# Performance work log

Hardware: AMD Instinct MI355X
Metric: run time of the kernel (lower is better)

The kernel has to match this reference:

```python
import jax, jax.numpy as jnp
import numpy as np

D_MODEL = 1024
H = 16
D_K = D_MODEL // H  # 64
B, S = 2, 2048


def setup_inputs() -> dict:
    key = jax.random.key(0)
    ks = jax.random.split(key, 8)
    scale = 1.0 / np.sqrt(D_MODEL)
    return {
        "q": jax.random.normal(ks[0], (B, S, D_MODEL), dtype=jnp.float32),
        "k": jax.random.normal(ks[1], (B, S, D_MODEL), dtype=jnp.float32),
        "v": jax.random.normal(ks[2], (B, S, D_MODEL), dtype=jnp.float32),
        "W_q": jax.random.normal(ks[3], (H, D_MODEL, D_K), dtype=jnp.float32) * scale,
        "W_k": jax.random.normal(ks[4], (H, D_MODEL, D_K), dtype=jnp.float32) * scale,
        "W_v": jax.random.normal(ks[5], (H, D_MODEL, D_K), dtype=jnp.float32) * scale,
        "W_o": jax.random.normal(ks[6], (D_MODEL, H * D_K), dtype=jnp.float32) * scale,
        "b_o": jnp.zeros((D_MODEL,), dtype=jnp.float32),
    }


def reference(q, k, v, W_q, W_k, W_v, W_o, b_o):
    b, s, _ = q.shape
    h, _, d_k = W_q.shape
    inv_sqrt_dk = jnp.asarray(1.0 / np.sqrt(d_k), q.dtype)
    # per-head projections: [b, h, s, d_k]
    qh = jnp.einsum("bsd,hdk->bhsk", q, W_q)
    kh = jnp.einsum("bsd,hdk->bhsk", k, W_k)
    vh = jnp.einsum("bsd,hdk->bhsk", v, W_v)
    # scaled dot product attention
    scores = jnp.einsum("bhqk,bhsk->bhqs", qh, kh) * inv_sqrt_dk  # [b,h,S,S]
    attn = jax.nn.softmax(scores, axis=-1)
    ctx = jnp.einsum("bhqs,bhsk->bhqk", attn, vh)  # [b,h,S,d_k]
    # chunk over heads + concat along feature dim -> [b, S, h*d_k], head-major
    ctx = ctx.transpose(0, 2, 1, 3).reshape(b, s, h * d_k)
    # final linear
    return ctx @ W_o.T + b_o
```

## Files before the change

### kernel.cpp

```cpp
#include <hip/hip_runtime.h>
#include <cstdint>
#include <cstddef>


typedef unsigned short bf16_t;
typedef __attribute__((ext_vector_type(8))) short short8;
typedef __attribute__((ext_vector_type(4))) float f32x4;

__device__ __forceinline__ uint32_t fbits(float f) {
  union { float f; uint32_t u; } v; v.f = f; return v.u;
}
__device__ __forceinline__ bf16_t f2bf(float f) {
  uint32_t u = fbits(f);
  return (bf16_t)((u + 0x7FFFu + ((u >> 16) & 1u)) >> 16);
}
__device__ __forceinline__ uint32_t packbf2(float lo, float hi) {
  uint32_t a = fbits(hi) + 0x8000u;
  uint32_t b = fbits(lo) + 0x8000u;
  return __builtin_amdgcn_perm(a, b, 0x07060302u);
}
__device__ __forceinline__ int4 cvt8(f32x4 lo, f32x4 hi) {
  return make_int4((int)packbf2(lo.x, lo.y), (int)packbf2(lo.z, lo.w),
                   (int)packbf2(hi.x, hi.y), (int)packbf2(hi.z, hi.w));
}

__global__ void prep_kernel(const float* __restrict__ Wo,
                            const float* __restrict__ Wq, const float* __restrict__ Wk,
                            const float* __restrict__ Wv,
                            bf16_t* __restrict__ Woo,
                            bf16_t* __restrict__ Wtq, bf16_t* __restrict__ Wtk,
                            bf16_t* __restrict__ Wtv) {
  int blk = blockIdx.x;
  int tid = threadIdx.x;
  if (blk < 1024) {
    int i = blk * 256 + tid;
    f32x4 val = ((const f32x4*)Wo)[i];
    ushort4 o;
    o.x = f2bf(val.x); o.y = f2bf(val.y); o.z = f2bf(val.z); o.w = f2bf(val.w);
    ((ushort4*)Woo)[i] = o;
  } else {
    int blk2 = blk - 1024;
    int z = blk2 >> 9, t = blk2 & 511;
    const float* W = z == 0 ? Wq : z == 1 ? Wk : Wv;
    bf16_t* Wt = z == 0 ? Wtq : z == 1 ? Wtk : Wtv;
    int h = t >> 5, d0 = (t & 31) * 32;
    __shared__ float tile[32][65];
    const float* src = W + ((size_t)h << 16) + (size_t)d0 * 64;
    int d = tid >> 3;
#pragma unroll
    for (int j = 0; j < 2; j++) {
      int dk = (tid & 7) * 8 + j * 4;
      *(f32x4*)&tile[d][dk] = *(const f32x4*)(src + d * 64 + dk);
    }
    __syncthreads();
    int dk2 = tid >> 2, c = tid & 3;
    union { ushort s[8]; int4 v; } o;
#pragma unroll
    for (int j = 0; j < 8; j++) o.s[j] = f2bf(tile[c * 8 + j][dk2]);
    *(int4*)(Wt + (size_t)(h * 64 + dk2) * 1024 + d0 + c * 8) = o.v;
  }
}

__global__ __launch_bounds__(256) void gemm_proj_kernel(
    const float* __restrict__ A0, const float* __restrict__ A1, const float* __restrict__ A2,
    const bf16_t* __restrict__ B0, const bf16_t* __restrict__ B1, const bf16_t* __restrict__ B2,
    bf16_t* __restrict__ O0, bf16_t* __restrict__ O1, bf16_t* __restrict__ O2,
    float s0)
{
  const int bid = blockIdx.x;
  const int nIdx = bid / 96;
  const int g = bid - nIdx * 96;
  const int z = g % 3;
  const int m0 = (g / 3) * 128, n0 = nIdx * 128;

  const float* A   = z == 0 ? A0 : z == 1 ? A1 : A2;
  const bf16_t* Bt = z == 0 ? B0 : z == 1 ? B1 : B2;
  bf16_t* Cout     = z == 0 ? O0 : z == 1 ? O1 : O2;
  const float scale = z == 0 ? s0 : 1.0f;
  const int K = 1024;

  __shared__ alignas(16) bf16_t smem[18432];

  const int tid = threadIdx.x;
  const int lane = tid & 63, wave = tid >> 6;
  const int wm = wave >> 1, wn = wave & 1;
  const int quad = lane >> 4, l15 = lane & 15;

  f32x4 acc[4][4];
#pragma unroll
  for (int i = 0; i < 4; i++)
#pragma unroll
    for (int j = 0; j < 4; j++) acc[i][j] = (f32x4)0.0f;

  const int c0 = wave * 128 + lane;
  const int c1 = c0 + 64;
  const float*  pa0 = A  + (size_t)(m0 + (c0 >> 2)) * K + (c0 & 3) * 8;
  const float*  pa1 = A  + (size_t)(m0 + (c1 >> 2)) * K + (c1 & 3) * 8;
  const bf16_t* pb0 = Bt + (size_t)(n0 + (c0 >> 2)) * K + (c0 & 3) * 8;
  const bf16_t* pb1 = Bt + (size_t)(n0 + (c1 >> 2)) * K + (c1 & 3) * 8;
  const int s0a = c0 * 8, s1a = c1 * 8;

  f32x4 ra0l = *(const f32x4*)pa0, ra0h = *(const f32x4*)(pa0 + 4);
  f32x4 ra1l = *(const f32x4*)pa1, ra1h = *(const f32x4*)(pa1 + 4);
  int4 rb0 = *(const int4*)pb0;
  int4 rb1 = *(const int4*)pb1;
  *(int4*)(smem + s0a) = cvt8(ra0l, ra0h);
  *(int4*)(smem + s1a) = cvt8(ra1l, ra1h);
  *(int4*)(smem + 4096 + s0a) = rb0;
  *(int4*)(smem + 4096 + s1a) = rb1;
  __syncthreads();

  for (int it = 0; it < 32; ++it) {
    const int co = (it & 1) * 8192;
    if (it < 31) {
      const int ko = (it + 1) * 32;
      ra0l = *(const f32x4*)(pa0 + ko); ra0h = *(const f32x4*)(pa0 + ko + 4);
      ra1l = *(const f32x4*)(pa1 + ko); ra1h = *(const f32x4*)(pa1 + ko + 4);
      rb0 = *(const int4*)(pb0 + ko);
      rb1 = *(const int4*)(pb1 + ko);
    }

    short8 af[4], bfr[4];
#pragma unroll
    for (int mi = 0; mi < 4; mi++)
      af[mi] = *(const short8*)(smem + co + (wm * 64 + mi * 16 + l15) * 32 + quad * 8);
#pragma unroll
    for (int ni = 0; ni < 4; ni++)
      bfr[ni] = *(const short8*)(smem + co + 4096 + (wn * 64 + ni * 16 + l15) * 32 + quad * 8);
#pragma unroll
    for (int mi = 0; mi < 4; mi++)
#pragma unroll
      for (int ni = 0; ni < 4; ni++)
        acc[mi][ni] = __builtin_amdgcn_mfma_f32_16x16x32_bf16(af[mi], bfr[ni], acc[mi][ni], 0, 0, 0);

    if (it < 31) {
      const int no = ((it + 1) & 1) * 8192;
      *(int4*)(smem + no + s0a) = cvt8(ra0l, ra0h);
      *(int4*)(smem + no + s1a) = cvt8(ra1l, ra1h);
      *(int4*)(smem + no + 4096 + s0a) = rb0;
      *(int4*)(smem + no + 4096 + s1a) = rb1;
    }
    __syncthreads();
  }

  const int s0r = m0 & 2047, bb = m0 >> 11, hp = n0 >> 6;
  if (z < 2) {
    bf16_t* slot = smem + wn * 9216;
#pragma unroll
    for (int ni = 0; ni < 4; ni++)
#pragma unroll
      for (int mi = 0; mi < 4; mi++)
#pragma unroll
        for (int r = 0; r < 4; r++)
          slot[(wm * 64 + mi * 16 + quad * 4 + r) * 72 + ni * 16 + l15] =
              f2bf(acc[mi][ni][r] * scale);
    __syncthreads();
#pragma unroll
    for (int rd = 0; rd < 8; ++rd) {
      int idx = rd * 256 + tid;
      int si = idx >> 10, mm = (idx >> 3) & 127, c8 = idx & 7;
      int4 val = *(const int4*)(smem + si * 9216 + mm * 72 + c8 * 8);
      *(int4*)(Cout + ((size_t)((bb * 16 + hp + si) * 2048 + s0r + mm)) * 64 + c8 * 8) = val;
    }
  } else {
    bf16_t* slot = smem + wn * 8704;
#pragma unroll
    for (int ni = 0; ni < 4; ni++)
#pragma unroll
      for (int mi = 0; mi < 4; mi++) {
        uint2 pk = make_uint2(packbf2(acc[mi][ni][0], acc[mi][ni][1]),
                              packbf2(acc[mi][ni][2], acc[mi][ni][3]));
        *(uint2*)(slot + (ni * 16 + l15) * 136 + wm * 64 + mi * 16 + quad * 4) = pk;
      }
    __syncthreads();
#pragma unroll
    for (int rd = 0; rd < 8; ++rd) {
      int idx = rd * 256 + tid;
      int si = idx >> 10, c = (idx >> 4) & 63, ck = idx & 15;
      int4 val = *(const int4*)(smem + si * 8704 + c * 136 + ck * 8);
      *(int4*)(Cout + (size_t)(bb * 16 + hp + si) * 131072 + (size_t)c * 2048 + s0r + ck * 8) = val;
    }
  }
}

__global__ __launch_bounds__(256) void gemm_out_kernel(
    const bf16_t* __restrict__ A, const bf16_t* __restrict__ Bt,
    float* __restrict__ C, const float* __restrict__ bias)
{
  const int K = 1024, N = 1024;
  __shared__ alignas(16) bf16_t smem[12288];
  const int tid = threadIdx.x;
  const int lane = tid & 63, wave = tid >> 6;
  const int quad = lane >> 4, l15 = lane & 15;
  const int m0 = (blockIdx.x & 31) * 128, n0 = (blockIdx.x >> 5) * 64;

  f32x4 acc[2][4];
#pragma unroll
  for (int i = 0; i < 2; i++)
#pragma unroll
    for (int j = 0; j < 4; j++) acc[i][j] = (f32x4)0.0f;

  const int c0 = wave * 128 + lane, c1 = c0 + 64;
  const int cb = wave * 64 + lane;
  const bf16_t* pa0 = A  + (size_t)(m0 + (c0 >> 2)) * K + (c0 & 3) * 8;
  const bf16_t* pa1 = A  + (size_t)(m0 + (c1 >> 2)) * K + (c1 & 3) * 8;
  const bf16_t* pb  = Bt + (size_t)(n0 + (cb >> 2)) * K + (cb & 3) * 8;
  const int s0a = c0 * 8, s1a = c1 * 8, sba = cb * 8;

  int4 ra0 = *(const int4*)pa0;
  int4 ra1 = *(const int4*)pa1;
  int4 rb  = *(const int4*)pb;
  *(int4*)(smem + s0a) = ra0;
  *(int4*)(smem + s1a) = ra1;
  *(int4*)(smem + 4096 + sba) = rb;
  __syncthreads();

  for (int it = 0; it < 32; ++it) {
    const int co = (it & 1) * 6144;
    if (it < 31) {
      const int ko = (it + 1) * 32;
      ra0 = *(const int4*)(pa0 + ko);
      ra1 = *(const int4*)(pa1 + ko);
      rb  = *(const int4*)(pb + ko);
    }

    short8 af[2], bfr[4];
#pragma unroll
    for (int mi = 0; mi < 2; mi++)
      af[mi] = *(const short8*)(smem + co + (wave * 32 + mi * 16 + l15) * 32 + quad * 8);
#pragma unroll
    for (int ni = 0; ni < 4; ni++)
      bfr[ni] = *(const short8*)(smem + co + 4096 + (ni * 16 + l15) * 32 + quad * 8);
#pragma unroll
    for (int mi = 0; mi < 2; mi++)
#pragma unroll
      for (int ni = 0; ni < 4; ni++)
        acc[mi][ni] = __builtin_amdgcn_mfma_f32_16x16x32_bf16(af[mi], bfr[ni], acc[mi][ni], 0, 0, 0);

    if (it < 31) {
      const int no = ((it + 1) & 1) * 6144;
      *(int4*)(smem + no + s0a) = ra0;
      *(int4*)(smem + no + s1a) = ra1;
      *(int4*)(smem + no + 4096 + sba) = rb;
    }
    __syncthreads();
  }

#pragma unroll
  for (int ni = 0; ni < 4; ni++) {
    int col = n0 + ni * 16 + l15;
    float bv = bias[col];
#pragma unroll
    for (int mi = 0; mi < 2; mi++) {
      int row = m0 + wave * 32 + mi * 16 + quad * 4;
#pragma unroll
      for (int r = 0; r < 4; r++)
        C[(size_t)(row + r) * N + col] = acc[mi][ni][r] + bv;
    }
  }
}

__global__ __launch_bounds__(512) void flash_kernel(
    const bf16_t* __restrict__ qh, const bf16_t* __restrict__ kh,
    const bf16_t* __restrict__ vT, bf16_t* __restrict__ ctx)
{
  __shared__ alignas(16) bf16_t KtF[2][4096];
  __shared__ alignas(16) bf16_t VtF[2][4096];
  __shared__ alignas(16) bf16_t PtF[16384];
  const int tid = threadIdx.x, lane = tid & 63, wave = tid >> 6;
  const int quad = lane >> 4, l15 = lane & 15;
  const int q0 = blockIdx.x * 256;
  const int h = blockIdx.y, b = blockIdx.z;
  const size_t headoff = (size_t)(b * 16 + h) * 2048 * 64;
  const bf16_t* Q = qh + headoff;
  const bf16_t* K = kh + headoff;
  const bf16_t* V = vT + headoff;

  short8 qf[2][2];
#pragma unroll
  for (int g = 0; g < 2; g++)
#pragma unroll
    for (int ks = 0; ks < 2; ks++)
      qf[g][ks] = *(const short8*)(Q + (size_t)(q0 + wave * 32 + g * 16 + l15) * 64
                                   + ks * 32 + quad * 8);

  f32x4 O[2][4];
#pragma unroll
  for (int g = 0; g < 2; g++)
#pragma unroll
    for (int mi = 0; mi < 4; mi++) O[g][mi] = (f32x4)0.0f;
  f32x4 lacc[2] = {(f32x4)0.0f, (f32x4)0.0f};

  const bf16_t* Kp = K + (size_t)((wave >> 1) * 16 + l15) * 64 + (wave & 1) * 32 + quad * 8;
  const bf16_t* Vp = V + (size_t)((wave >> 1) * 16 + l15) * 2048 + (wave & 1) * 32 + quad * 8;
  const int soff = wave * 512 + lane * 8;
  const int pwb = wave * 4096 + ((quad >> 1) * 16 + l15) * 16 + 8 * (quad & 1);

  auto body = [&](int buf) {
    f32x4 S[2][4];
#pragma unroll
    for (int g = 0; g < 2; g++)
#pragma unroll
      for (int mi = 0; mi < 4; mi++) S[g][mi] = (f32x4)0.0f;
#pragma unroll
    for (int ks = 0; ks < 2; ks++) {
#pragma unroll
      for (int mi = 0; mi < 4; mi++) {
        short8 kf = *(const short8*)(&KtF[buf][(mi * 2 + ks) * 512 + lane * 8]);
        S[0][mi] = __builtin_amdgcn_mfma_f32_16x16x32_bf16(kf, qf[0][ks], S[0][mi], 0, 0, 0);
        S[1][mi] = __builtin_amdgcn_mfma_f32_16x16x32_bf16(kf, qf[1][ks], S[1][mi], 0, 0, 0);
      }
    }
#pragma unroll
    for (int g = 0; g < 2; g++) {
#pragma unroll
      for (int mi = 0; mi < 4; mi++)
#pragma unroll
        for (int r = 0; r < 4; r++)
          S[g][mi][r] = __builtin_amdgcn_exp2f(S[g][mi][r]);
      lacc[g] += (S[g][0] + S[g][1]) + (S[g][2] + S[g][3]);
    }
#pragma unroll
    for (int g = 0; g < 2; g++)
#pragma unroll
      for (int mi = 0; mi < 4; mi++) {
        uint2 pk = make_uint2(packbf2(S[g][mi][0], S[g][mi][1]),
                              packbf2(S[g][mi][2], S[g][mi][3]));
        *(uint2*)((char*)PtF + pwb + g * 2048 + (mi >> 1) * 1024 + (mi & 1) * 512) = pk;
      }
#pragma unroll
    for (int ks = 0; ks < 2; ks++) {
      short8 pf0 = *(const short8*)(&PtF[wave * 2048 + (ks * 64 + lane) * 8]);
      short8 pf1 = *(const short8*)(&PtF[wave * 2048 + 1024 + (ks * 64 + lane) * 8]);
#pragma unroll
      for (int mi = 0; mi < 4; mi++) {
        short8 vf = *(const short8*)(&VtF[buf][(mi * 2 + ks) * 512 + lane * 8]);
        O[0][mi] = __builtin_amdgcn_mfma_f32_16x16x32_bf16(vf, pf0, O[0][mi], 0, 0, 0);
        O[1][mi] = __builtin_amdgcn_mfma_f32_16x16x32_bf16(vf, pf1, O[1][mi], 0, 0, 0);
      }
    }
  };

  int4 k0 = *(const int4*)Kp, v0 = *(const int4*)Vp;
  *(int4*)(&KtF[0][soff]) = k0;
  *(int4*)(&VtF[0][soff]) = v0;
  int4 kA = *(const int4*)(Kp + 4096), vA = *(const int4*)(Vp + 64);
  __syncthreads();

  for (int it = 0; it < 32; it += 2) {
    *(int4*)(&KtF[1][soff]) = kA;
    *(int4*)(&VtF[1][soff]) = vA;
    int4 kB, vB;
    if (it + 2 < 32) {
      kB = *(const int4*)(Kp + (size_t)(it + 2) * 4096);
      vB = *(const int4*)(Vp + (size_t)(it + 2) * 64);
    }
    body(0);
    __syncthreads();

    if (it + 2 < 32) {
      *(int4*)(&KtF[0][soff]) = kB;
      *(int4*)(&VtF[0][soff]) = vB;
    }
    if (it + 3 < 32) {
      kA = *(const int4*)(Kp + (size_t)(it + 3) * 4096);
      vA = *(const int4*)(Vp + (size_t)(it + 3) * 64);
    }
    body(1);
    __syncthreads();
  }

#pragma unroll
  for (int g = 0; g < 2; g++) {
    float l = (lacc[g][0] + lacc[g][1]) + (lacc[g][2] + lacc[g][3]);
    l += __shfl_xor(l, 16, 64);
    l += __shfl_xor(l, 32, 64);
    float inv = 1.0f / l;
    int qrow = q0 + wave * 32 + g * 16 + l15;
    bf16_t* crow = ctx + ((size_t)(b * 2048 + qrow)) * 1024 + h * 64;
#pragma unroll
    for (int mi = 0; mi < 4; mi++) {
      uint2 pk = make_uint2(packbf2(O[g][mi][0] * inv, O[g][mi][1] * inv),
                            packbf2(O[g][mi][2] * inv, O[g][mi][3] * inv));
      *(uint2*)(crow + mi * 16 + quad * 4) = pk;
    }
  }
}

extern "C" void kernel_launch(void* const* d_in, const int* in_sizes, int n_in,
                              void* d_out, int out_size, void* d_ws, size_t ws_size,
                              hipStream_t stream)
{
  const float* q  = (const float*)d_in[0];
  const float* k  = (const float*)d_in[1];
  const float* v  = (const float*)d_in[2];
  const float* Wq = (const float*)d_in[3];
  const float* Wk = (const float*)d_in[4];
  const float* Wv = (const float*)d_in[5];
  const float* Wo = (const float*)d_in[6];
  const float* bo = (const float*)d_in[7];
  float* out = (float*)d_out;

  const size_t NX = (size_t)4096 * 1024;
  const size_t NW = (size_t)1024 * 1024;

  char* p = (char*)d_ws;
  bf16_t* Wtq = (bf16_t*)p; p += NW * 2;
  bf16_t* Wtk = (bf16_t*)p; p += NW * 2;
  bf16_t* Wtv = (bf16_t*)p; p += NW * 2;
  bf16_t* Wob = (bf16_t*)p; p += NW * 2;
  bf16_t* qhb = (bf16_t*)p; p += NX * 2;
  bf16_t* khb = (bf16_t*)p; p += NX * 2;
  bf16_t* vTb = (bf16_t*)p; p += NX * 2;
  bf16_t* ctxb = (bf16_t*)p; p += NX * 2;

  prep_kernel<<<2560, 256, 0, stream>>>(Wo, Wq, Wk, Wv, Wob, Wtq, Wtk, Wtv);

  const float qscale = 0.125f * 1.44269504088896340736f;
  gemm_proj_kernel<<<768, 256, 0, stream>>>(q, k, v, Wtq, Wtk, Wtv,
                                            qhb, khb, vTb, qscale);

  flash_kernel<<<dim3(8, 16, 2), 512, 0, stream>>>(qhb, khb, vTb, ctxb);

  gemm_out_kernel<<<512, 256, 0, stream>>>(ctxb, Wob, out, bo);

  (void)in_sizes; (void)n_in; (void)out_size; (void)ws_size;
}
```

Before: 210.5 us.

## Use direct global-to-LDS loads, pre-convert activations to bf16, reshape flash grid

Activations q/k/v are converted to bf16 in the prep kernel so the projection GEMM streams bf16. The GEMMs and the flash kernel now fill shared memory with global_load_lds instead of register staging. The flash kernel moves from 512-thread blocks over 256 query rows to 256-thread blocks over 128 rows on a flattened 512-block grid, and raises wave priority around the MFMA sections. The extra conversion pass adds global traffic and workspace. The direct LDS loads change the order of data in shared memory, so correctness depends on the new lane mapping matching the fragment reads.

```diff
diff --git a/kernel.cpp b/kernel.cpp
--- a/kernel.cpp
+++ b/kernel.cpp
@@ -24,12 +24,22 @@
                    (int)packbf2(hi.x, hi.y), (int)packbf2(hi.z, hi.w));
 }
 
+__device__ __forceinline__ void gload16(const bf16_t* g, bf16_t* l) {
+  __builtin_amdgcn_global_load_lds(
+      (const __attribute__((address_space(1))) void*)g,
+      (__attribute__((address_space(3))) void*)l, 16, 0, 0);
+}
+
 __global__ void prep_kernel(const float* __restrict__ Wo,
                             const float* __restrict__ Wq, const float* __restrict__ Wk,
                             const float* __restrict__ Wv,
+                            const float* __restrict__ q, const float* __restrict__ k,
+                            const float* __restrict__ v,
                             bf16_t* __restrict__ Woo,
                             bf16_t* __restrict__ Wtq, bf16_t* __restrict__ Wtk,
-                            bf16_t* __restrict__ Wtv) {
+                            bf16_t* __restrict__ Wtv,
+                            bf16_t* __restrict__ qb, bf16_t* __restrict__ kb,
+                            bf16_t* __restrict__ vb) {
   int blk = blockIdx.x;
   int tid = threadIdx.x;
   if (blk < 1024) {
@@ -38,7 +48,7 @@
     ushort4 o;
     o.x = f2bf(val.x); o.y = f2bf(val.y); o.z = f2bf(val.z); o.w = f2bf(val.w);
     ((ushort4*)Woo)[i] = o;
-  } else {
+  } else if (blk < 2560) {
     int blk2 = blk - 1024;
     int z = blk2 >> 9, t = blk2 & 511;
     const float* W = z == 0 ? Wq : z == 1 ? Wk : Wv;
@@ -58,11 +68,21 @@
 #pragma unroll
     for (int j = 0; j < 8; j++) o.s[j] = f2bf(tile[c * 8 + j][dk2]);
     *(int4*)(Wt + (size_t)(h * 64 + dk2) * 1024 + d0 + c * 8) = o.v;
+  } else {
+    int blk3 = blk - 2560;
+    int z = blk3 >> 11;
+    int t3 = blk3 & 2047;
+    const float* src = z == 0 ? q : z == 1 ? k : v;
+    bf16_t* dst = z == 0 ? qb : z == 1 ? kb : vb;
+    int i = t3 * 256 + tid;
+    f32x4 lo = ((const f32x4*)src)[i * 2];
+    f32x4 hi = ((const f32x4*)src)[i * 2 + 1];
+    ((int4*)dst)[i] = cvt8(lo, hi);
   }
 }
 
 __global__ __launch_bounds__(256) void gemm_proj_kernel(
-    const float* __restrict__ A0, const float* __restrict__ A1, const float* __restrict__ A2,
+    const bf16_t* __restrict__ A0, const bf16_t* __restrict__ A1, const bf16_t* __restrict__ A2,
     const bf16_t* __restrict__ B0, const bf16_t* __restrict__ B1, const bf16_t* __restrict__ B2,
     bf16_t* __restrict__ O0, bf16_t* __restrict__ O1, bf16_t* __restrict__ O2,
     float s0)
@@ -73,7 +93,7 @@
   const int z = g % 3;
   const int m0 = (g / 3) * 128, n0 = nIdx * 128;
 
-  const float* A   = z == 0 ? A0 : z == 1 ? A1 : A2;
+  const bf16_t* A  = z == 0 ? A0 : z == 1 ? A1 : A2;
   const bf16_t* Bt = z == 0 ? B0 : z == 1 ? B1 : B2;
   bf16_t* Cout     = z == 0 ? O0 : z == 1 ? O1 : O2;
   const float scale = z == 0 ? s0 : 1.0f;
@@ -92,54 +112,43 @@
 #pragma unroll
     for (int j = 0; j < 4; j++) acc[i][j] = (f32x4)0.0f;
 
-  const int c0 = wave * 128 + lane;
-  const int c1 = c0 + 64;
-  const float*  pa0 = A  + (size_t)(m0 + (c0 >> 2)) * K + (c0 & 3) * 8;
-  const float*  pa1 = A  + (size_t)(m0 + (c1 >> 2)) * K + (c1 & 3) * 8;
-  const bf16_t* pb0 = Bt + (size_t)(n0 + (c0 >> 2)) * K + (c0 & 3) * 8;
-  const bf16_t* pb1 = Bt + (size_t)(n0 + (c1 >> 2)) * K + (c1 & 3) * 8;
-  const int s0a = c0 * 8, s1a = c1 * 8;
-
-  f32x4 ra0l = *(const f32x4*)pa0, ra0h = *(const f32x4*)(pa0 + 4);
-  f32x4 ra1l = *(const f32x4*)pa1, ra1h = *(const f32x4*)(pa1 + 4);
-  int4 rb0 = *(const int4*)pb0;
-  int4 rb1 = *(const int4*)pb1;
-  *(int4*)(smem + s0a) = cvt8(ra0l, ra0h);
-  *(int4*)(smem + s1a) = cvt8(ra1l, ra1h);
-  *(int4*)(smem + 4096 + s0a) = rb0;
-  *(int4*)(smem + 4096 + s1a) = rb1;
+  const int srow = tid >> 2, scol = (tid & 3) * 8;
+  const bf16_t* pa0 = A  + (size_t)(m0 + srow) * K + scol;
+  const bf16_t* pa1 = pa0 + (size_t)64 * K;
+  const bf16_t* pb0 = Bt + (size_t)(n0 + srow) * K + scol;
+  const bf16_t* pb1 = pb0 + (size_t)64 * K;
+  const int lws = wave * 512;
+
+  gload16(pa0, smem + lws);
+  gload16(pa1, smem + 2048 + lws);
+  gload16(pb0, smem + 4096 + lws);
+  gload16(pb1, smem + 6144 + lws);
   __syncthreads();
 
   for (int it = 0; it < 32; ++it) {
-    const int co = (it & 1) * 8192;
+    const int cur = (it & 1) * 8192;
     if (it < 31) {
+      const int nxt = ((it + 1) & 1) * 8192;
       const int ko = (it + 1) * 32;
-      ra0l = *(const f32x4*)(pa0 + ko); ra0h = *(const f32x4*)(pa0 + ko + 4);
-      ra1l = *(const f32x4*)(pa1 + ko); ra1h = *(const f32x4*)(pa1 + ko + 4);
-      rb0 = *(const int4*)(pb0 + ko);
-      rb1 = *(const int4*)(pb1 + ko);
+      gload16(pa0 + ko, smem + nxt + lws);
+      gload16(pa1 + ko, smem + nxt + 2048 + lws);
+      gload16(pb0 + ko, smem + nxt + 4096 + lws);
+      gload16(pb1 + ko, smem + nxt + 6144 + lws);
     }
 
     short8 af[4], bfr[4];
 #pragma unroll
     for (int mi = 0; mi < 4; mi++)
-      af[mi] = *(const short8*)(smem + co + (wm * 64 + mi * 16 + l15) * 32 + quad * 8);
+      af[mi] = *(const short8*)(smem + cur + (wm * 64 + mi * 16 + l15) * 32 + quad * 8);
 #pragma unroll
     for (int ni = 0; ni < 4; ni++)
-      bfr[ni] = *(const short8*)(smem + co + 4096 + (wn * 64 + ni * 16 + l15) * 32 + quad * 8);
+      bfr[ni] = *(const short8*)(smem + cur + 4096 + (wn * 64 + ni * 16 + l15) * 32 + quad * 8);
 #pragma unroll
     for (int mi = 0; mi < 4; mi++)
 #pragma unroll
       for (int ni = 0; ni < 4; ni++)
         acc[mi][ni] = __builtin_amdgcn_mfma_f32_16x16x32_bf16(af[mi], bfr[ni], acc[mi][ni], 0, 0, 0);
 
-    if (it < 31) {
-      const int no = ((it + 1) & 1) * 8192;
-      *(int4*)(smem + no + s0a) = cvt8(ra0l, ra0h);
-      *(int4*)(smem + no + s1a) = cvt8(ra1l, ra1h);
-      *(int4*)(smem + no + 4096 + s0a) = rb0;
-      *(int4*)(smem + no + 4096 + s1a) = rb1;
-    }
     __syncthreads();
   }
 
@@ -200,49 +209,40 @@
 #pragma unroll
     for (int j = 0; j < 4; j++) acc[i][j] = (f32x4)0.0f;
 
-  const int c0 = wave * 128 + lane, c1 = c0 + 64;
-  const int cb = wave * 64 + lane;
-  const bf16_t* pa0 = A  + (size_t)(m0 + (c0 >> 2)) * K + (c0 & 3) * 8;
-  const bf16_t* pa1 = A  + (size_t)(m0 + (c1 >> 2)) * K + (c1 & 3) * 8;
-  const bf16_t* pb  = Bt + (size_t)(n0 + (cb >> 2)) * K + (cb & 3) * 8;
-  const int s0a = c0 * 8, s1a = c1 * 8, sba = cb * 8;
-
-  int4 ra0 = *(const int4*)pa0;
-  int4 ra1 = *(const int4*)pa1;
-  int4 rb  = *(const int4*)pb;
-  *(int4*)(smem + s0a) = ra0;
-  *(int4*)(smem + s1a) = ra1;
-  *(int4*)(smem + 4096 + sba) = rb;
+  const int srow = tid >> 2, scol = (tid & 3) * 8;
+  const bf16_t* pa0 = A  + (size_t)(m0 + srow) * K + scol;
+  const bf16_t* pa1 = pa0 + (size_t)64 * K;
+  const bf16_t* pb  = Bt + (size_t)(n0 + srow) * K + scol;
+  const int lws = wave * 512;
+
+  gload16(pa0, smem + lws);
+  gload16(pa1, smem + 2048 + lws);
+  gload16(pb,  smem + 4096 + lws);
   __syncthreads();
 
   for (int it = 0; it < 32; ++it) {
-    const int co = (it & 1) * 6144;
+    const int cur = (it & 1) * 6144;
     if (it < 31) {
+      const int nxt = ((it + 1) & 1) * 6144;
       const int ko = (it + 1) * 32;
-      ra0 = *(const int4*)(pa0 + ko);
-      ra1 = *(const int4*)(pa1 + ko);
-      rb  = *(const int4*)(pb + ko);
+      gload16(pa0 + ko, smem + nxt + lws);
+      gload16(pa1 + ko, smem + nxt + 2048 + lws);
+      gload16(pb + ko,  smem + nxt + 4096 + lws);
     }
 
     short8 af[2], bfr[4];
 #pragma unroll
     for (int mi = 0; mi < 2; mi++)
-      af[mi] = *(const short8*)(smem + co + (wave * 32 + mi * 16 + l15) * 32 + quad * 8);
+      af[mi] = *(const short8*)(smem + cur + (wave * 32 + mi * 16 + l15) * 32 + quad * 8);
 #pragma unroll
     for (int ni = 0; ni < 4; ni++)
-      bfr[ni] = *(const short8*)(smem + co + 4096 + (ni * 16 + l15) * 32 + quad * 8);
+      bfr[ni] = *(const short8*)(smem + cur + 4096 + (ni * 16 + l15) * 32 + quad * 8);
 #pragma unroll
     for (int mi = 0; mi < 2; mi++)
 #pragma unroll
       for (int ni = 0; ni < 4; ni++)
         acc[mi][ni] = __builtin_amdgcn_mfma_f32_16x16x32_bf16(af[mi], bfr[ni], acc[mi][ni], 0, 0, 0);
 
-    if (it < 31) {
-      const int no = ((it + 1) & 1) * 6144;
-      *(int4*)(smem + no + s0a) = ra0;
-      *(int4*)(smem + no + s1a) = ra1;
-      *(int4*)(smem + no + 4096 + sba) = rb;
-    }
     __syncthreads();
   }
 
@@ -260,18 +260,20 @@
   }
 }
 
-__global__ __launch_bounds__(512) void flash_kernel(
+__global__ __launch_bounds__(256) void flash_kernel(
     const bf16_t* __restrict__ qh, const bf16_t* __restrict__ kh,
     const bf16_t* __restrict__ vT, bf16_t* __restrict__ ctx)
 {
   __shared__ alignas(16) bf16_t KtF[2][4096];
   __shared__ alignas(16) bf16_t VtF[2][4096];
-  __shared__ alignas(16) bf16_t PtF[16384];
+  __shared__ alignas(16) bf16_t PtF[8192];
   const int tid = threadIdx.x, lane = tid & 63, wave = tid >> 6;
   const int quad = lane >> 4, l15 = lane & 15;
-  const int q0 = blockIdx.x * 256;
-  const int h = blockIdx.y, b = blockIdx.z;
-  const size_t headoff = (size_t)(b * 16 + h) * 2048 * 64;
+  const int gid = blockIdx.x;
+  const int hb = gid & 31;
+  const int h = hb & 15, b = hb >> 4;
+  const int q0 = (gid >> 5) * 128;
+  const size_t headoff = (size_t)hb * 2048 * 64;
   const bf16_t* Q = qh + headoff;
   const bf16_t* K = kh + headoff;
   const bf16_t* V = vT + headoff;
@@ -293,8 +295,15 @@
 
   const bf16_t* Kp = K + (size_t)((wave >> 1) * 16 + l15) * 64 + (wave & 1) * 32 + quad * 8;
   const bf16_t* Vp = V + (size_t)((wave >> 1) * 16 + l15) * 2048 + (wave & 1) * 32 + quad * 8;
-  const int soff = wave * 512 + lane * 8;
+  const int lws = wave * 512;
   const int pwb = wave * 4096 + ((quad >> 1) * 16 + l15) * 16 + 8 * (quad & 1);
+
+  auto stage = [&](int buf, int t) {
+    gload16(Kp + (size_t)t * 4096,        &KtF[buf][lws]);
+    gload16(Kp + (size_t)t * 4096 + 2048, &KtF[buf][lws + 2048]);
+    gload16(Vp + (size_t)t * 64,          &VtF[buf][lws]);
+    gload16(Vp + (size_t)t * 64 + 65536,  &VtF[buf][lws + 2048]);
+  };
 
   auto body = [&](int buf) {
     f32x4 S[2][4];
@@ -302,6 +311,7 @@
     for (int g = 0; g < 2; g++)
 #pragma unroll
       for (int mi = 0; mi < 4; mi++) S[g][mi] = (f32x4)0.0f;
+    __builtin_amdgcn_s_setprio(1);
 #pragma unroll
     for (int ks = 0; ks < 2; ks++) {
 #pragma unroll
@@ -311,6 +321,7 @@
         S[1][mi] = __builtin_amdgcn_mfma_f32_16x16x32_bf16(kf, qf[1][ks], S[1][mi], 0, 0, 0);
       }
     }
+    __builtin_amdgcn_s_setprio(0);
 #pragma unroll
     for (int g = 0; g < 2; g++) {
 #pragma unroll
@@ -328,6 +339,7 @@
                               packbf2(S[g][mi][2], S[g][mi][3]));
         *(uint2*)((char*)PtF + pwb + g * 2048 + (mi >> 1) * 1024 + (mi & 1) * 512) = pk;
       }
+    __builtin_amdgcn_s_setprio(1);
 #pragma unroll
     for (int ks = 0; ks < 2; ks++) {
       short8 pf0 = *(const short8*)(&PtF[wave * 2048 + (ks * 64 + lane) * 8]);
@@ -339,34 +351,14 @@
         O[1][mi] = __builtin_amdgcn_mfma_f32_16x16x32_bf16(vf, pf1, O[1][mi], 0, 0, 0);
       }
     }
+    __builtin_amdgcn_s_setprio(0);
   };
 
-  int4 k0 = *(const int4*)Kp, v0 = *(const int4*)Vp;
-  *(int4*)(&KtF[0][soff]) = k0;
-  *(int4*)(&VtF[0][soff]) = v0;
-  int4 kA = *(const int4*)(Kp + 4096), vA = *(const int4*)(Vp + 64);
+  stage(0, 0);
   __syncthreads();
-
-  for (int it = 0; it < 32; it += 2) {
-    *(int4*)(&KtF[1][soff]) = kA;
-    *(int4*)(&VtF[1][soff]) = vA;
-    int4 kB, vB;
-    if (it + 2 < 32) {
-      kB = *(const int4*)(Kp + (size_t)(it + 2) * 4096);
-      vB = *(const int4*)(Vp + (size_t)(it + 2) * 64);
-    }
-    body(0);
-    __syncthreads();
-
-    if (it + 2 < 32) {
-      *(int4*)(&KtF[0][soff]) = kB;
-      *(int4*)(&VtF[0][soff]) = vB;
-    }
-    if (it + 3 < 32) {
-      kA = *(const int4*)(Kp + (size_t)(it + 3) * 4096);
-      vA = *(const int4*)(Vp + (size_t)(it + 3) * 64);
-    }
-    body(1);
+  for (int it = 0; it < 32; ++it) {
+    if (it < 31) stage((it + 1) & 1, it + 1);
+    body(it & 1);
     __syncthreads();
   }
 
@@ -409,18 +401,22 @@
   bf16_t* Wtk = (bf16_t*)p; p += NW * 2;
   bf16_t* Wtv = (bf16_t*)p; p += NW * 2;
   bf16_t* Wob = (bf16_t*)p; p += NW * 2;
+  bf16_t* qb  = (bf16_t*)p; p += NX * 2;
+  bf16_t* kb  = (bf16_t*)p; p += NX * 2;
+  bf16_t* vb  = (bf16_t*)p; p += NX * 2;
   bf16_t* qhb = (bf16_t*)p; p += NX * 2;
   bf16_t* khb = (bf16_t*)p; p += NX * 2;
   bf16_t* vTb = (bf16_t*)p; p += NX * 2;
   bf16_t* ctxb = (bf16_t*)p; p += NX * 2;
 
-  prep_kernel<<<2560, 256, 0, stream>>>(Wo, Wq, Wk, Wv, Wob, Wtq, Wtk, Wtv);
+  prep_kernel<<<8704, 256, 0, stream>>>(Wo, Wq, Wk, Wv, q, k, v,
+                                        Wob, Wtq, Wtk, Wtv, qb, kb, vb);
 
   const float qscale = 0.125f * 1.44269504088896340736f;
-  gemm_proj_kernel<<<768, 256, 0, stream>>>(q, k, v, Wtq, Wtk, Wtv,
+  gemm_proj_kernel<<<768, 256, 0, stream>>>(qb, kb, vb, Wtq, Wtk, Wtv,
                                             qhb, khb, vTb, qscale);
 
-  flash_kernel<<<dim3(8, 16, 2), 512, 0, stream>>>(qhb, khb, vTb, ctxb);
+  flash_kernel<<<512, 256, 0, stream>>>(qhb, khb, vTb, ctxb);
 
   gemm_out_kernel<<<512, 256, 0, stream>>>(ctxb, Wob, out, bo);
 
```

New measurement: 217.6 us. 3.4% more time.
